# Optimization experiments

Hardware: AMD Instinct MI355X
Metric: run time of the kernel (lower is better)

## Reference

```python
import jax, jax.numpy as jnp
import numpy as np

B, T, I, H, O = 256, 512, 64, 256, 16
THRESH = 1.0

def _xavier(key, fan_out, fan_in):
    bound = float(np.sqrt(6.0 / (fan_in + fan_out)))
    return jax.random.uniform(key, (fan_out, fan_in), jnp.float32, -bound, bound)

def setup_inputs() -> dict:
    key = jax.random.key(0)
    k = jax.random.split(key, 4)
    return {
        "x": jax.random.normal(k[0], (B, T, I), jnp.float32),
        "W_i2h": _xavier(k[1], H, I),
        "b_i2h": jnp.zeros((H,), jnp.float32),
        "W_h2h": 0.001 * jax.random.normal(k[2], (H, H), jnp.float32),  # trunc_normal std=0.001 approx
        "b_h2h": jnp.zeros((H,), jnp.float32),
        "W_out": _xavier(k[3], O, H),
        "b_out": jnp.zeros((O,), jnp.float32),
        "hidden_init": jnp.zeros((1, H), jnp.float32),
    }

def reference(x, W_i2h, b_i2h, W_h2h, b_h2h, W_out, b_out, hidden_init):
    # Precompute input projection for all timesteps in one GEMM: [B,T,H]
    xi = jnp.einsum('bti,hi->bth', x, W_i2h) + b_i2h
    h0 = jnp.tile(hidden_init, (x.shape[0], 1))  # [B,H]

    def step(h, xt):
        pre = h + xt + h @ W_h2h.T + b_h2h
        a = jnp.minimum(jax.nn.relu(pre), jnp.float32(THRESH))
        return a, a

    hidden, rnn_out_t = jax.lax.scan(step, h0, jnp.swapaxes(xi, 0, 1))  # [T,B,H]
    rnn_out = jnp.swapaxes(rnn_out_t, 0, 1)  # [B,T,H]
    output = rnn_out @ W_out.T + b_out  # [B,T,O]
    return (output, hidden, rnn_out)
```

## Files before the change

### kernel.cpp

```cpp
#include <hip/hip_runtime.h>

#define NB 256
#define NT 512
#define NI 64
#define NH 256
#define NO 16

typedef __attribute__((ext_vector_type(8))) short short8;
typedef __attribute__((ext_vector_type(8))) __bf16 bf16x8;
typedef __attribute__((ext_vector_type(4))) float f32x4;
typedef __attribute__((ext_vector_type(4))) int int4v;

__device__ __forceinline__ unsigned short f2bf(float f) {
  unsigned u = __builtin_bit_cast(unsigned, f);
  u += 0x7fffu + ((u >> 16) & 1u);
  return (unsigned short)(u >> 16);
}

__device__ __forceinline__ f32x4 mfma16(short8 a, short8 b, f32x4 c) {
  return __builtin_amdgcn_mfma_f32_16x16x32_bf16(
      __builtin_bit_cast(bf16x8, a), __builtin_bit_cast(bf16x8, b), c, 0, 0, 0);
}

__device__ __forceinline__ int4v mfma_i8(int4v a, int4v b, int4v c) {
  return __builtin_amdgcn_mfma_i32_16x16x64_i8(a, b, c, 0, 0, 0);
}

__device__ __forceinline__ short8 pack8v(f32x4 lo, f32x4 hi) {
  short8 r;
#pragma unroll
  for (int i = 0; i < 4; ++i) {
    r[i]     = (short)f2bf(lo[i]);
    r[i + 4] = (short)f2bf(hi[i]);
  }
  return r;
}

__device__ __forceinline__ short8 pack8(const float* __restrict__ p) {
  return pack8v(*reinterpret_cast<const f32x4*>(p),
                *reinterpret_cast<const f32x4*>(p + 4));
}

__device__ __forceinline__ void step_barrier() {
  asm volatile("s_waitcnt lgkmcnt(0)" ::: "memory");
  __builtin_amdgcn_s_barrier();
  asm volatile("" ::: "memory");
}

__global__ __launch_bounds__(512, 2)
void rnn_fused(const float* __restrict__ x,  const float* __restrict__ Wi,
               const float* __restrict__ bi, const float* __restrict__ Wh,
               const float* __restrict__ bh, const float* __restrict__ Wo,
               const float* __restrict__ bo, const float* __restrict__ h0,
               float* __restrict__ dout)
{
  const int b   = blockIdx.x;
  const int tid = threadIdx.x;
  const int w   = tid >> 6;
  const int l   = tid & 63;
  const int lg  = l >> 4;
  const int ll  = l & 15;

  __shared__ __align__(16) signed char    hq[2][256];
  __shared__ __align__(16) unsigned short rnnwin[16 * NH];
  __shared__ __align__(16) float          xi_lds[NH][20];

  float* outp = dout;
  float* hidp = dout + (size_t)NB * NT * NO;
  float* rnnp = hidp + (size_t)NB * NH;

  const f32x4 cz = {0.f, 0.f, 0.f, 0.f};
  const int4v iz = {0, 0, 0, 0};

  int4v whq[2][4];
  float dq[2];
#pragma unroll
  for (int jt = 0; jt < 2; ++jt) {
    const int j = w * 32 + jt * 16 + ll;
    const float* wr = Wh + (size_t)j * NH;
    float m = 0.f;
#pragma unroll
    for (int kt = 0; kt < 4; ++kt)
#pragma unroll
      for (int e4 = 0; e4 < 4; ++e4) {
        f32x4 v = *reinterpret_cast<const f32x4*>(wr + kt * 64 + lg * 16 + e4 * 4);
#pragma unroll
        for (int i = 0; i < 4; ++i) m = fmaxf(m, fabsf(v[i]));
      }
    m = fmaxf(m, __shfl_xor(m, 16));
    m = fmaxf(m, __shfl_xor(m, 32));
    const float inv = (m > 0.f) ? 127.f / m : 0.f;
    dq[jt] = m / (127.f * 127.f);
#pragma unroll
    for (int kt = 0; kt < 4; ++kt) {
      unsigned u[4] = {0u, 0u, 0u, 0u};
#pragma unroll
      for (int e = 0; e < 16; ++e) {
        const float v = wr[kt * 64 + lg * 16 + e] * inv;
        int q = (int)(v + (v >= 0.f ? 0.5f : -0.5f));
        q = q > 127 ? 127 : (q < -127 ? -127 : q);
        u[e >> 2] |= ((unsigned)(q & 255)) << (8 * (e & 3));
      }
      int4v t; t[0] = (int)u[0]; t[1] = (int)u[1]; t[2] = (int)u[2]; t[3] = (int)u[3];
      whq[jt][kt] = t;
    }
  }

  short8 wif[2][2];
#pragma unroll
  for (int jt = 0; jt < 2; ++jt) {
    const int j = w * 32 + jt * 16 + ll;
#pragma unroll
    for (int kx = 0; kx < 2; ++kx)
      wif[jt][kx] = pack8(Wi + (size_t)j * NI + kx * 32 + lg * 8);
  }
  short8 woA[8];
#pragma unroll
  for (int kt = 0; kt < 8; ++kt)
    woA[kt] = pack8(Wo + (size_t)ll * NH + kt * 32 + lg * 8);

  float breg[2];
  breg[0] = bi[w * 32 + ll]      + bh[w * 32 + ll];
  breg[1] = bi[w * 32 + 16 + ll] + bh[w * 32 + 16 + ll];
  const float bout = bo[ll];

  float h_reg0 = h0[w * 32 + ll];
  float h_reg1 = h0[w * 32 + 16 + ll];

  const int  jw   = w * 32 + lg * 16 + ll;
  const int  widx = ((jw >> 6) << 6) | (((jw >> 4) & 3) << 4) | (jw & 15);
  const bool wr_act = (lg < 2);

  if (tid < 256) {
    const int jj = tid;
    const int wi2 = ((jj >> 6) << 6) | (((jj >> 4) & 3) << 4) | (jj & 15);
    float hv = fminf(fmaxf(h0[jj], -1.f), 1.f);
    hq[0][wi2] = (signed char)(int)(hv * 127.f + (hv >= 0.f ? 0.5f : -0.5f));
  }

  const float* xrow = x + (size_t)b * NT * NI + (size_t)ll * NI + lg * 8;
  f32x4 xpre[4];
  xpre[0] = *reinterpret_cast<const f32x4*>(xrow);
  xpre[1] = *reinterpret_cast<const f32x4*>(xrow + 4);
  xpre[2] = *reinterpret_cast<const f32x4*>(xrow + 32);
  xpre[3] = *reinterpret_cast<const f32x4*>(xrow + 36);

  __syncthreads();

  const int j0 = w * 32 + ll;
  const int j1 = w * 32 + 16 + ll;

  auto outproj = [&](int tbase) {
    f32x4 oacc = cz;
#pragma unroll
    for (int kt = 0; kt < 8; ++kt) {
      const char* ap = (const char*)rnnwin + ll * 512 +
                       ((kt * 64 + lg * 16) ^ (ll << 4));
      short8 af = *reinterpret_cast<const short8*>(ap);
      oacc = mfma16(af, woA[kt], oacc);
    }
#pragma unroll
    for (int r = 0; r < 4; ++r) {
      const int tp = lg * 4 + r;
      outp[((size_t)b * NT + tbase - 16 + tp) * NO + ll] = oacc[r] + bout;
    }
  };

#pragma unroll 1
  for (int t0 = 0; t0 < NT; t0 += 16) {
    if (t0 > 0 && w == 0) outproj(t0);
    {
      short8 xf0 = pack8v(xpre[0], xpre[1]);
      short8 xf1 = pack8v(xpre[2], xpre[3]);
#pragma unroll
      for (int jt = 0; jt < 2; ++jt) {
        f32x4 acc = mfma16(xf0, wif[jt][0], cz);
        acc = mfma16(xf1, wif[jt][1], acc);
        const int j = w * 32 + jt * 16 + ll;
        *(f32x4*)&xi_lds[j][lg * 4] = acc;
      }
    }
    if (t0 + 16 < NT) {
      const float* xp = x + (size_t)b * NT * NI + (size_t)(t0 + 16 + ll) * NI + lg * 8;
      xpre[0] = *reinterpret_cast<const f32x4*>(xp);
      xpre[1] = *reinterpret_cast<const f32x4*>(xp + 4);
      xpre[2] = *reinterpret_cast<const f32x4*>(xp + 32);
      xpre[3] = *reinterpret_cast<const f32x4*>(xp + 36);
    }
    step_barrier();

#pragma unroll 1
    for (int q4 = 0; q4 < 4; ++q4) {
      const int tb = t0 + q4 * 4;
      f32x4 xiA = *(const f32x4*)&xi_lds[j0][q4 * 4];
      f32x4 xiB = *(const f32x4*)&xi_lds[j1][q4 * 4];

#define STEP(TT, SUB)                                                          \
      {                                                                        \
        const int t    = (TT);                                                 \
        const int trow = t & 15;                                               \
        const int p    = t & 1;                                                \
        int4v ha[4];                                                           \
        _Pragma("unroll")                                                      \
        for (int kt = 0; kt < 4; ++kt)                                         \
          ha[kt] = *(const int4v*)&hq[p][kt * 64 + lg * 16];                   \
        int4v acc0 = mfma_i8(ha[0], whq[0][0], iz);                            \
        int4v acc1 = mfma_i8(ha[0], whq[1][0], iz);                            \
        _Pragma("unroll")                                                      \
        for (int kt = 1; kt < 4; ++kt) {                                       \
          acc0 = mfma_i8(ha[kt], whq[0][kt], acc0);                            \
          acc1 = mfma_i8(ha[kt], whq[1][kt], acc1);                            \
        }                                                                      \
        const float a0 = fminf(fmaxf(                                          \
            (float)acc0[0] * dq[0] + h_reg0 + xiA[SUB] + breg[0], 0.f), 1.f);  \
        const float a1 = fminf(fmaxf(                                          \
            (float)acc1[0] * dq[1] + h_reg1 + xiB[SUB] + breg[1], 0.f), 1.f);  \
        h_reg0 = a0; h_reg1 = a1;                                              \
        if (wr_act) {                                                          \
          const float aw = lg ? a1 : a0;                                       \
          hq[p ^ 1][widx] = (signed char)(int)(aw * 127.f + 0.5f);             \
          const int byte = trow * 512 + ((2 * jw) ^ (trow << 4));              \
          rnnwin[byte >> 1] = f2bf(aw);                                        \
          rnnp[((size_t)b * NT + t) * NH + jw] = aw;                           \
        }                                                                      \
        step_barrier();                                                        \
      }

      STEP(tb + 0, 0)
      STEP(tb + 1, 1)
      STEP(tb + 2, 2)
      STEP(tb + 3, 3)
#undef STEP
    }
  }

  if (w == 0) outproj(NT);
  if (wr_act) {
    const float aw = lg ? h_reg1 : h_reg0;
    hidp[(size_t)b * NH + jw] = aw;
  }
}

extern "C" void kernel_launch(void* const* d_in, const int* in_sizes, int n_in,
                              void* d_out, int out_size, void* d_ws, size_t ws_size,
                              hipStream_t stream) {
  const float* x  = (const float*)d_in[0];
  const float* Wi = (const float*)d_in[1];
  const float* bi = (const float*)d_in[2];
  const float* Wh = (const float*)d_in[3];
  const float* bh = (const float*)d_in[4];
  const float* Wo = (const float*)d_in[5];
  const float* bo = (const float*)d_in[6];
  const float* h0 = (const float*)d_in[7];
  rnn_fused<<<dim3(NB), dim3(512), 0, stream>>>(x, Wi, bi, Wh, bh, Wo, bo, h0,
                                                (float*)d_out);
}
```

Baseline: 169.8 us.

## Quantize recurrent matvec to FP4 and use scaled f8f6f4 MFMA

The recurrent h@W_h2h product moves from int8 MFMA (4 K-steps of 16x16x64) to FP4 (e2m1) MFMA with the 16x16x128 scaled instruction, so each step needs only 2 MFMAs per output tile. The hidden state is packed two values per byte, using a shuffle to pair neighbouring lanes, which halves the LDS traffic on the serial critical path. FP4 quantization is far coarser than int8 and risks numerical error against the reference, and the extra shuffle plus the piecewise encoding add latency to each step.

```diff
diff --git a/kernel.cpp b/kernel.cpp
--- a/kernel.cpp
+++ b/kernel.cpp
@@ -10,6 +10,7 @@
 typedef __attribute__((ext_vector_type(8))) __bf16 bf16x8;
 typedef __attribute__((ext_vector_type(4))) float f32x4;
 typedef __attribute__((ext_vector_type(4))) int int4v;
+typedef __attribute__((ext_vector_type(8))) int int8v;
 
 __device__ __forceinline__ unsigned short f2bf(float f) {
   unsigned u = __builtin_bit_cast(unsigned, f);
@@ -22,8 +23,20 @@
       __builtin_bit_cast(bf16x8, a), __builtin_bit_cast(bf16x8, b), c, 0, 0, 0);
 }
 
-__device__ __forceinline__ int4v mfma_i8(int4v a, int4v b, int4v c) {
-  return __builtin_amdgcn_mfma_i32_16x16x64_i8(a, b, c, 0, 0, 0);
+__device__ __forceinline__ f32x4 mfma_fp4(int8v a, int8v b, f32x4 c) {
+  return __builtin_amdgcn_mfma_scale_f32_16x16x128_f8f6f4(
+      a, b, c, 4, 4, 0, 0x7f7f7f7f, 0, 0x7f7f7f7f);
+}
+
+__device__ __forceinline__ int fp4s(float v) {
+  const float m = fabsf(v);
+  int c;
+  if (m < 1.75f)      c = (int)(m * 2.f + 0.5f);
+  else if (m < 2.5f)  c = 4;
+  else if (m < 3.5f)  c = 5;
+  else if (m < 5.0f)  c = 6;
+  else                c = 7;
+  return c | (v < 0.f ? 8 : 0);
 }
 
 __device__ __forceinline__ short8 pack8v(f32x4 lo, f32x4 hi) {
@@ -61,7 +74,7 @@
   const int lg  = l >> 4;
   const int ll  = l & 15;
 
-  __shared__ __align__(16) signed char    hq[2][256];
+  __shared__ __align__(16) unsigned char  hq4[2][128];
   __shared__ __align__(16) unsigned short rnnwin[16 * NH];
   __shared__ __align__(16) float          xi_lds[NH][20];
 
@@ -70,9 +83,8 @@
   float* rnnp = hidp + (size_t)NB * NH;
 
   const f32x4 cz = {0.f, 0.f, 0.f, 0.f};
-  const int4v iz = {0, 0, 0, 0};
-
-  int4v whq[2][4];
+
+  int8v wq8[2][2];
   float dq[2];
 #pragma unroll
   for (int jt = 0; jt < 2; ++jt) {
@@ -80,29 +92,27 @@
     const float* wr = Wh + (size_t)j * NH;
     float m = 0.f;
 #pragma unroll
-    for (int kt = 0; kt < 4; ++kt)
-#pragma unroll
-      for (int e4 = 0; e4 < 4; ++e4) {
-        f32x4 v = *reinterpret_cast<const f32x4*>(wr + kt * 64 + lg * 16 + e4 * 4);
+    for (int kc = 0; kc < 2; ++kc)
+#pragma unroll
+      for (int e4 = 0; e4 < 8; ++e4) {
+        f32x4 v = *reinterpret_cast<const f32x4*>(wr + kc * 128 + lg * 32 + e4 * 4);
 #pragma unroll
         for (int i = 0; i < 4; ++i) m = fmaxf(m, fabsf(v[i]));
       }
     m = fmaxf(m, __shfl_xor(m, 16));
     m = fmaxf(m, __shfl_xor(m, 32));
-    const float inv = (m > 0.f) ? 127.f / m : 0.f;
-    dq[jt] = m / (127.f * 127.f);
-#pragma unroll
-    for (int kt = 0; kt < 4; ++kt) {
+    const float s = (m > 0.f) ? 6.f / m : 0.f;
+    dq[jt] = m * (1.f / 36.f);
+#pragma unroll
+    for (int kc = 0; kc < 2; ++kc) {
       unsigned u[4] = {0u, 0u, 0u, 0u};
 #pragma unroll
-      for (int e = 0; e < 16; ++e) {
-        const float v = wr[kt * 64 + lg * 16 + e] * inv;
-        int q = (int)(v + (v >= 0.f ? 0.5f : -0.5f));
-        q = q > 127 ? 127 : (q < -127 ? -127 : q);
-        u[e >> 2] |= ((unsigned)(q & 255)) << (8 * (e & 3));
-      }
-      int4v t; t[0] = (int)u[0]; t[1] = (int)u[1]; t[2] = (int)u[2]; t[3] = (int)u[3];
-      whq[jt][kt] = t;
+      for (int e = 0; e < 32; ++e) {
+        const int code = fp4s(wr[kc * 128 + lg * 32 + e] * s);
+        u[e >> 3] |= ((unsigned)code) << (4 * (e & 7));
+      }
+      int8v t = {(int)u[0], (int)u[1], (int)u[2], (int)u[3], 0, 0, 0, 0};
+      wq8[jt][kc] = t;
     }
   }
 
@@ -127,15 +137,13 @@
   float h_reg0 = h0[w * 32 + ll];
   float h_reg1 = h0[w * 32 + 16 + ll];
 
-  const int  jw   = w * 32 + lg * 16 + ll;
-  const int  widx = ((jw >> 6) << 6) | (((jw >> 4) & 3) << 4) | (jw & 15);
+  const int  jw     = w * 32 + lg * 16 + ll;
   const bool wr_act = (lg < 2);
 
-  if (tid < 256) {
-    const int jj = tid;
-    const int wi2 = ((jj >> 6) << 6) | (((jj >> 4) & 3) << 4) | (jj & 15);
-    float hv = fminf(fmaxf(h0[jj], -1.f), 1.f);
-    hq[0][wi2] = (signed char)(int)(hv * 127.f + (hv >= 0.f ? 0.5f : -0.5f));
+  if (tid < 128) {
+    const int q0 = fp4s(h0[2 * tid]     * 6.f);
+    const int q1 = fp4s(h0[2 * tid + 1] * 6.f);
+    hq4[0][tid] = (unsigned char)(q0 | (q1 << 4));
   }
 
   const float* xrow = x + (size_t)b * NT * NI + (size_t)ll * NI + lg * 8;
@@ -200,25 +208,25 @@
         const int t    = (TT);                                                 \
         const int trow = t & 15;                                               \
         const int p    = t & 1;                                                \
-        int4v ha[4];                                                           \
-        _Pragma("unroll")                                                      \
-        for (int kt = 0; kt < 4; ++kt)                                         \
-          ha[kt] = *(const int4v*)&hq[p][kt * 64 + lg * 16];                   \
-        int4v acc0 = mfma_i8(ha[0], whq[0][0], iz);                            \
-        int4v acc1 = mfma_i8(ha[0], whq[1][0], iz);                            \
-        _Pragma("unroll")                                                      \
-        for (int kt = 1; kt < 4; ++kt) {                                       \
-          acc0 = mfma_i8(ha[kt], whq[0][kt], acc0);                            \
-          acc1 = mfma_i8(ha[kt], whq[1][kt], acc1);                            \
-        }                                                                      \
-        const float a0 = fminf(fmaxf(                                          \
-            (float)acc0[0] * dq[0] + h_reg0 + xiA[SUB] + breg[0], 0.f), 1.f);  \
-        const float a1 = fminf(fmaxf(                                          \
-            (float)acc1[0] * dq[1] + h_reg1 + xiB[SUB] + breg[1], 0.f), 1.f);  \
+        int4v h4a = *(const int4v*)&hq4[p][lg * 16];                           \
+        int4v h4b = *(const int4v*)&hq4[p][64 + lg * 16];                      \
+        int8v A0 = {h4a[0], h4a[1], h4a[2], h4a[3], 0, 0, 0, 0};               \
+        int8v A1 = {h4b[0], h4b[1], h4b[2], h4b[3], 0, 0, 0, 0};               \
+        const float hxi0 = h_reg0 + xiA[SUB] + breg[0];                        \
+        const float hxi1 = h_reg1 + xiB[SUB] + breg[1];                        \
+        f32x4 acc0 = mfma_fp4(A0, wq8[0][0], cz);                              \
+        f32x4 acc1 = mfma_fp4(A0, wq8[1][0], cz);                              \
+        acc0 = mfma_fp4(A1, wq8[0][1], acc0);                                  \
+        acc1 = mfma_fp4(A1, wq8[1][1], acc1);                                  \
+        const float a0 = fminf(fmaxf(fmaf(acc0[0], dq[0], hxi0), 0.f), 1.f);   \
+        const float a1 = fminf(fmaxf(fmaf(acc1[0], dq[1], hxi1), 0.f), 1.f);   \
         h_reg0 = a0; h_reg1 = a1;                                              \
+        const float aw = lg ? a1 : a0;                                         \
+        const int   qn = fp4s(aw * 6.f);                                       \
+        const int   qp = __shfl_xor(qn, 1);                                    \
         if (wr_act) {                                                          \
-          const float aw = lg ? a1 : a0;                                       \
-          hq[p ^ 1][widx] = (signed char)(int)(aw * 127.f + 0.5f);             \
+          if (!(ll & 1))                                                       \
+            hq4[p ^ 1][jw >> 1] = (unsigned char)(qn | (qp << 4));             \
           const int byte = trow * 512 + ((2 * jw) ^ (trow << 4));              \
           rnnwin[byte >> 1] = f2bf(aw);                                        \
           rnnp[((size_t)b * NT + t) * NH + jw] = aw;                           \
```

After: 311.2 us. +83.3%, slower.

## Shorten recurrent step critical path and rotate output projection across waves

Applied to the files above, without the earlier changes.

The recurrent step now splits the int8 MFMA accumulation into two independent chains, folds both biases into the precomputed input projection, and uses fmaf plus fmed3 for the clamp. It also fully unrolls the 16-step block so all xi values are loaded once. The output projection rotates across waves instead of always running on wave 0, and its weights are reloaded from global memory on each call rather than held in registers. Together these aim to cut per-step latency and even out the load across waves, at the cost of extra global loads for W_out and larger code.

```diff
diff --git a/kernel.cpp b/kernel.cpp
--- a/kernel.cpp
+++ b/kernel.cpp
@@ -8,6 +8,7 @@
 
 typedef __attribute__((ext_vector_type(8))) short short8;
 typedef __attribute__((ext_vector_type(8))) __bf16 bf16x8;
+typedef __attribute__((ext_vector_type(2))) float f32x2;
 typedef __attribute__((ext_vector_type(4))) float f32x4;
 typedef __attribute__((ext_vector_type(4))) int int4v;
 
@@ -107,32 +108,26 @@
   }
 
   short8 wif[2][2];
+  float bregW[2];
 #pragma unroll
   for (int jt = 0; jt < 2; ++jt) {
     const int j = w * 32 + jt * 16 + ll;
 #pragma unroll
     for (int kx = 0; kx < 2; ++kx)
       wif[jt][kx] = pack8(Wi + (size_t)j * NI + kx * 32 + lg * 8);
-  }
-  short8 woA[8];
-#pragma unroll
-  for (int kt = 0; kt < 8; ++kt)
-    woA[kt] = pack8(Wo + (size_t)ll * NH + kt * 32 + lg * 8);
-
-  float breg[2];
-  breg[0] = bi[w * 32 + ll]      + bh[w * 32 + ll];
-  breg[1] = bi[w * 32 + 16 + ll] + bh[w * 32 + 16 + ll];
+    bregW[jt] = bi[j] + bh[j];
+  }
   const float bout = bo[ll];
 
   float h_reg0 = h0[w * 32 + ll];
   float h_reg1 = h0[w * 32 + 16 + ll];
 
-  const int  jw   = w * 32 + lg * 16 + ll;
-  const int  widx = ((jw >> 6) << 6) | (((jw >> 4) & 3) << 4) | (jw & 15);
+  const int  jw     = w * 32 + lg * 16 + ll;
+  const int  widx   = ((jw >> 6) << 6) | (((jw >> 4) & 3) << 4) | (jw & 15);
   const bool wr_act = (lg < 2);
 
   if (tid < 256) {
-    const int jj = tid;
+    const int jj  = tid;
     const int wi2 = ((jj >> 6) << 6) | (((jj >> 4) & 3) << 4) | (jj & 15);
     float hv = fminf(fmaxf(h0[jj], -1.f), 1.f);
     hq[0][wi2] = (signed char)(int)(hv * 127.f + (hv >= 0.f ? 0.5f : -0.5f));
@@ -154,10 +149,11 @@
     f32x4 oacc = cz;
 #pragma unroll
     for (int kt = 0; kt < 8; ++kt) {
+      short8 wo = pack8(Wo + (size_t)ll * NH + kt * 32 + lg * 8);
       const char* ap = (const char*)rnnwin + ll * 512 +
                        ((kt * 64 + lg * 16) ^ (ll << 4));
       short8 af = *reinterpret_cast<const short8*>(ap);
-      oacc = mfma16(af, woA[kt], oacc);
+      oacc = mfma16(af, wo, oacc);
     }
 #pragma unroll
     for (int r = 0; r < 4; ++r) {
@@ -166,9 +162,44 @@
     }
   };
 
+#define STEP(TT, XIV0, XIV1)                                                   \
+  {                                                                            \
+    const int t    = (TT);                                                     \
+    const int trow = t & 15;                                                   \
+    const int p    = t & 1;                                                    \
+    int4v ha[4];                                                               \
+    _Pragma("unroll")                                                          \
+    for (int kt = 0; kt < 4; ++kt)                                             \
+      ha[kt] = *(const int4v*)&hq[p][kt * 64 + lg * 16];                       \
+                  \
+    int4v a0a = mfma_i8(ha[0], whq[0][0], iz);                                 \
+    int4v a0b = mfma_i8(ha[2], whq[0][2], iz);                                 \
+    int4v a1a = mfma_i8(ha[0], whq[1][0], iz);                                 \
+    int4v a1b = mfma_i8(ha[2], whq[1][2], iz);                                 \
+    a0a = mfma_i8(ha[1], whq[0][1], a0a);                                     \
+    a0b = mfma_i8(ha[3], whq[0][3], a0b);                                     \
+    a1a = mfma_i8(ha[1], whq[1][1], a1a);                                     \
+    a1b = mfma_i8(ha[3], whq[1][3], a1b);                                     \
+    const float hx0 = h_reg0 + (XIV0);                    \
+    const float hx1 = h_reg1 + (XIV1);                                         \
+    const float s0 = (float)(a0a[0] + a0b[0]);                                 \
+    const float s1 = (float)(a1a[0] + a1b[0]);                                 \
+    const float a0 = __builtin_amdgcn_fmed3f(fmaf(s0, dq[0], hx0), 0.f, 1.f);  \
+    const float a1 = __builtin_amdgcn_fmed3f(fmaf(s1, dq[1], hx1), 0.f, 1.f);  \
+    h_reg0 = a0; h_reg1 = a1;                                                  \
+    if (wr_act) {                                                              \
+      const float aw = lg ? a1 : a0;                                           \
+      hq[p ^ 1][widx] = (signed char)(int)(aw * 127.f + 0.5f);                 \
+      const int byte = trow * 512 + ((2 * jw) ^ (trow << 4));                  \
+      rnnwin[byte >> 1] = f2bf(aw);                                            \
+      rnnp[((size_t)b * NT + t) * NH + jw] = aw;                               \
+    }                                                                          \
+    step_barrier();                                                            \
+  }
+
 #pragma unroll 1
   for (int t0 = 0; t0 < NT; t0 += 16) {
-    if (t0 > 0 && w == 0) outproj(t0);
+    if (t0 > 0 && w == (((t0 >> 4) - 1) & 7)) outproj(t0);
     {
       short8 xf0 = pack8v(xpre[0], xpre[1]);
       short8 xf1 = pack8v(xpre[2], xpre[3]);
@@ -177,7 +208,10 @@
         f32x4 acc = mfma16(xf0, wif[jt][0], cz);
         acc = mfma16(xf1, wif[jt][1], acc);
         const int j = w * 32 + jt * 16 + ll;
-        *(f32x4*)&xi_lds[j][lg * 4] = acc;
+        f32x4 xo;
+#pragma unroll
+        for (int r = 0; r < 4; ++r) xo[r] = acc[r] + bregW[jt];
+        *(f32x4*)&xi_lds[j][lg * 4] = xo;
       }
     }
     if (t0 + 16 < NT) {
@@ -189,52 +223,25 @@
     }
     step_barrier();
 
-#pragma unroll 1
-    for (int q4 = 0; q4 < 4; ++q4) {
-      const int tb = t0 + q4 * 4;
-      f32x4 xiA = *(const f32x4*)&xi_lds[j0][q4 * 4];
-      f32x4 xiB = *(const f32x4*)&xi_lds[j1][q4 * 4];
-
-#define STEP(TT, SUB)                                                          \
-      {                                                                        \
-        const int t    = (TT);                                                 \
-        const int trow = t & 15;                                               \
-        const int p    = t & 1;                                                \
-        int4v ha[4];                                                           \
-        _Pragma("unroll")                                                      \
-        for (int kt = 0; kt < 4; ++kt)                                         \
-          ha[kt] = *(const int4v*)&hq[p][kt * 64 + lg * 16];                   \
-        int4v acc0 = mfma_i8(ha[0], whq[0][0], iz);                            \
-        int4v acc1 = mfma_i8(ha[0], whq[1][0], iz);                            \
-        _Pragma("unroll")                                                      \
-        for (int kt = 1; kt < 4; ++kt) {                                       \
-          acc0 = mfma_i8(ha[kt], whq[0][kt], acc0);                            \
-          acc1 = mfma_i8(ha[kt], whq[1][kt], acc1);                            \
-        }                                                                      \
-        const float a0 = fminf(fmaxf(                                          \
-            (float)acc0[0] * dq[0] + h_reg0 + xiA[SUB] + breg[0], 0.f), 1.f);  \
-        const float a1 = fminf(fmaxf(                                          \
-            (float)acc1[0] * dq[1] + h_reg1 + xiB[SUB] + breg[1], 0.f), 1.f);  \
-        h_reg0 = a0; h_reg1 = a1;                                              \
-        if (wr_act) {                                                          \
-          const float aw = lg ? a1 : a0;                                       \
-          hq[p ^ 1][widx] = (signed char)(int)(aw * 127.f + 0.5f);             \
-          const int byte = trow * 512 + ((2 * jw) ^ (trow << 4));              \
-          rnnwin[byte >> 1] = f2bf(aw);                                        \
-          rnnp[((size_t)b * NT + t) * NH + jw] = aw;                           \
-        }                                                                      \
-        step_barrier();                                                        \
-      }
-
-      STEP(tb + 0, 0)
-      STEP(tb + 1, 1)
-      STEP(tb + 2, 2)
-      STEP(tb + 3, 3)
+    f32x4 xqA[4], xqB[4];
+#pragma unroll
+    for (int q = 0; q < 4; ++q) {
+      xqA[q] = *(const f32x4*)&xi_lds[j0][q * 4];
+      xqB[q] = *(const f32x4*)&xi_lds[j1][q * 4];
+    }
+
+    STEP(t0 + 0,  xqA[0][0], xqB[0][0]) STEP(t0 + 1,  xqA[0][1], xqB[0][1])
+    STEP(t0 + 2,  xqA[0][2], xqB[0][2]) STEP(t0 + 3,  xqA[0][3], xqB[0][3])
+    STEP(t0 + 4,  xqA[1][0], xqB[1][0]) STEP(t0 + 5,  xqA[1][1], xqB[1][1])
+    STEP(t0 + 6,  xqA[1][2], xqB[1][2]) STEP(t0 + 7,  xqA[1][3], xqB[1][3])
+    STEP(t0 + 8,  xqA[2][0], xqB[2][0]) STEP(t0 + 9,  xqA[2][1], xqB[2][1])
+    STEP(t0 + 10, xqA[2][2], xqB[2][2]) STEP(t0 + 11, xqA[2][3], xqB[2][3])
+    STEP(t0 + 12, xqA[3][0], xqB[3][0]) STEP(t0 + 13, xqA[3][1], xqB[3][1])
+    STEP(t0 + 14, xqA[3][2], xqB[3][2]) STEP(t0 + 15, xqA[3][3], xqB[3][3])
+  }
 #undef STEP
-    }
-  }
-
-  if (w == 0) outproj(NT);
+
+  if (w == 7) outproj(NT);
   if (wr_act) {
     const float aw = lg ? h_reg1 : h_reg0;
     hidp[(size_t)b * NH + jw] = aw;
```

Result: slower. 189.7 us (+11.7%).
